# Optimization experiments

Measured on AMD Instinct MI355X. Metric: run time of the kernel, lower is better.

The kernel has to match this reference:

```python
import jax, jax.numpy as jnp
import numpy as np

D = 1024      # input_dim
H = 4096      # expert_hidden_dim
C = 512       # num_classes
E = 8         # num_experts
K = 2         # top_k
B = 16384     # batch
LN_EPS = 1e-5


def setup_inputs() -> dict:
    key = jax.random.key(0)
    ks = jax.random.split(key, 6)
    scale = 0.02
    return {
        "x": jax.random.normal(ks[0], (B, D), dtype=jnp.float32),
        "gate_w": jax.random.normal(ks[1], (D, E), dtype=jnp.float32) * scale,
        "gate_b": jnp.zeros((E,), dtype=jnp.float32),
        "w1": jax.random.normal(ks[2], (E, D, H), dtype=jnp.float32) * scale,
        "b1": jnp.zeros((E, H), dtype=jnp.float32),
        "ln_g": jnp.ones((E, H), dtype=jnp.float32),
        "ln_b": jnp.zeros((E, H), dtype=jnp.float32),
        "w2": jax.random.normal(ks[3], (E, H, C), dtype=jnp.float32) * scale,
        "b2": jnp.zeros((E, C), dtype=jnp.float32),
    }


def reference(x, gate_w, gate_b, w1, b1, ln_g, ln_b, w2, b2):
    # Router: logits [B,E], top-k over experts, softmax over the k selected logits
    logits = x @ gate_w + gate_b
    top_vals, top_idx = jax.lax.top_k(logits, K)        # [B,K]
    probs = jax.nn.softmax(top_vals, axis=1)            # [B,K]

    # Combined gate weight per (token, expert): replaces the nested k/expert
    # mask-gather-scatter loops; top_idx rows have distinct experts, so this
    # is exactly sum_k probs[:,k] * (top_idx[:,k]==e). [B,E]
    n = x.shape[0]
    weight = jnp.zeros((n, E), dtype=x.dtype).at[jnp.arange(n)[:, None], top_idx].add(probs)

    out = jnp.zeros((n, C), dtype=x.dtype)
    for e in range(E):  # fixed small expert count; each expert has distinct params
        h = x @ w1[e] + b1[e]                           # [B,H]
        mu = jnp.mean(h, axis=-1, keepdims=True)
        var = jnp.var(h, axis=-1, keepdims=True)
        h = (h - mu) * jax.lax.rsqrt(var + LN_EPS) * ln_g[e] + ln_b[e]
        h = jax.nn.gelu(h, approximate=False)           # torch GELU default = erf
        # Dropout is identity in eval mode.
        out = out + weight[:, e:e + 1] * (h @ w2[e] + b2[e])
    return out, logits
```

## Files before the change

kernel.cpp:

```cpp
#include <hip/hip_runtime.h>
#include <hip/hip_bf16.h>
#include <cstdint>

#define DEV __device__ __forceinline__

constexpr int Bt = 16384;
constexpr int Dd = 1024;
constexpr int Hh = 4096;
constexpr int Cc = 512;
constexpr int Ee = 8;
constexpr int PCAP = 34816;

typedef short bf16x8 __attribute__((ext_vector_type(8)));
typedef ushort u16x8 __attribute__((ext_vector_type(8)));
typedef float f32x4  __attribute__((ext_vector_type(4)));

DEV ushort f2bf(float f){
  uint32_t u = __float_as_uint(f);
  u += 0x7fffu + ((u >> 16) & 1u);
  return (ushort)(u >> 16);
}
DEV float bf2f(ushort u){ return __uint_as_float(((uint32_t)u) << 16); }

DEV float gelu_t(float x){
  float x2 = x * x;
  float z = x * (0.7978845608f + 0.0356774081f * x2);
  float t = __builtin_amdgcn_exp2f(z * -2.8853900818f);
  return x * __builtin_amdgcn_rcpf(1.f + t);
}

typedef const __attribute__((address_space(1))) void* gptr_t;
typedef __attribute__((address_space(3))) void* lptr_t;
DEV void gload_lds16(const void* g, void* l){
  __builtin_amdgcn_global_load_lds((gptr_t)g, (lptr_t)l, 16, 0, 0);
}

#define BARRIER() __builtin_amdgcn_s_barrier()
#define WAITL(N) do { asm volatile("s_waitcnt lgkmcnt(" #N ")" ::: "memory"); \
                      __builtin_amdgcn_sched_barrier(0); } while(0)
#define WAITV(N) asm volatile("s_waitcnt vmcnt(" #N ")" ::: "memory")

__global__ __launch_bounds__(256) void k_router(
    const float* __restrict__ x, const float* __restrict__ gw,
    const float* __restrict__ gb, float* __restrict__ logits,
    int2* __restrict__ topi, float2* __restrict__ topp)
{
  __shared__ float lgwT[Ee * Dd];
  int tid = threadIdx.x;
  const float4* gw4 = (const float4*)gw;
  for (int i = tid; i < Dd * Ee / 4; i += 256){
    float4 v = gw4[i];
    int d = i >> 1, e0 = (i & 1) * 4;
    lgwT[(e0 + 0) * Dd + d] = v.x;
    lgwT[(e0 + 1) * Dd + d] = v.y;
    lgwT[(e0 + 2) * Dd + d] = v.z;
    lgwT[(e0 + 3) * Dd + d] = v.w;
  }
  __syncthreads();
  int wv = tid >> 6, lane = tid & 63;
  int t = blockIdx.x * 4 + wv;
  const float* xr = x + (size_t)t * Dd;
  float acc[Ee];
  #pragma unroll
  for (int e = 0; e < Ee; e++) acc[e] = 0.f;
  for (int i = 0; i < Dd / 64; i++){
    int d = i * 64 + lane;
    float xs = xr[d];
    #pragma unroll
    for (int e = 0; e < Ee; e++) acc[e] += xs * lgwT[e * Dd + d];
  }
  #pragma unroll
  for (int e = 0; e < Ee; e++){
    #pragma unroll
    for (int m = 1; m < 64; m <<= 1) acc[e] += __shfl_xor(acc[e], m, 64);
  }
  if (lane == 0){
    float lg[Ee];
    #pragma unroll
    for (int e = 0; e < Ee; e++) lg[e] = acc[e] + gb[e];
    #pragma unroll
    for (int e = 0; e < Ee; e++) logits[(size_t)t * Ee + e] = lg[e];
    int i0 = 0; float v0 = lg[0];
    #pragma unroll
    for (int e = 1; e < Ee; e++) if (lg[e] > v0){ v0 = lg[e]; i0 = e; }
    int i1 = (i0 == 0) ? 1 : 0; float v1 = lg[i1];
    #pragma unroll
    for (int e = 0; e < Ee; e++) if (e != i0 && lg[e] > v1){ v1 = lg[e]; i1 = e; }
    float ex = expf(v1 - v0);
    float p0 = 1.f / (1.f + ex);
    float p1 = ex * p0;
    topi[t] = make_int2(i0, i1);
    topp[t] = make_float2(p0, p1);
  }
}

__global__ __launch_bounds__(256) void k_offsets(
    const int2* __restrict__ topi, int* __restrict__ off)
{
  __shared__ int part[4][8];
  int tid = threadIdx.x, lane = tid & 63, w = tid >> 6;
  int c0 = 0, c1 = 0, c2 = 0, c3 = 0, c4 = 0, c5 = 0, c6 = 0, c7 = 0;
  for (int t = tid; t < Bt; t += 256){
    int2 ii = topi[t];
    c0 += (ii.x == 0) + (ii.y == 0);
    c1 += (ii.x == 1) + (ii.y == 1);
    c2 += (ii.x == 2) + (ii.y == 2);
    c3 += (ii.x == 3) + (ii.y == 3);
    c4 += (ii.x == 4) + (ii.y == 4);
    c5 += (ii.x == 5) + (ii.y == 5);
    c6 += (ii.x == 6) + (ii.y == 6);
    c7 += (ii.x == 7) + (ii.y == 7);
  }
  #pragma unroll
  for (int m = 1; m < 64; m <<= 1){
    c0 += __shfl_xor(c0, m, 64); c1 += __shfl_xor(c1, m, 64);
    c2 += __shfl_xor(c2, m, 64); c3 += __shfl_xor(c3, m, 64);
    c4 += __shfl_xor(c4, m, 64); c5 += __shfl_xor(c5, m, 64);
    c6 += __shfl_xor(c6, m, 64); c7 += __shfl_xor(c7, m, 64);
  }
  if (lane == 0){
    part[w][0] = c0; part[w][1] = c1; part[w][2] = c2; part[w][3] = c3;
    part[w][4] = c4; part[w][5] = c5; part[w][6] = c6; part[w][7] = c7;
  }
  __syncthreads();
  if (tid == 0){
    int a = 0;
    for (int e = 0; e < Ee; e++){
      int h = part[0][e] + part[1][e] + part[2][e] + part[3][e];
      off[e] = a; a += ((h + 255) >> 8) << 8;
    }
    off[Ee] = a;
  }
}

__global__ __launch_bounds__(256) void k_scatter(
    const int2* __restrict__ topi, const int* __restrict__ off,
    int* __restrict__ fill, int* __restrict__ ptok, int2* __restrict__ pidx)
{
  __shared__ int lcnt[8], lbase[8];
  int tid = threadIdx.x;
  if (tid < 8) lcnt[tid] = 0;
  __syncthreads();
  int t = blockIdx.x * 256 + tid;
  int2 ii = topi[t];
  int r0 = atomicAdd(&lcnt[ii.x], 1);
  int r1 = atomicAdd(&lcnt[ii.y], 1);
  __syncthreads();
  if (tid < 8) lbase[tid] = off[tid] + atomicAdd(&fill[tid], lcnt[tid]);
  __syncthreads();
  int p0 = lbase[ii.x] + r0;
  int p1 = lbase[ii.y] + r1;
  ptok[p0] = t;
  ptok[p1] = t;
  pidx[t] = make_int2(p0, p1);
}

__global__ __launch_bounds__(256) void k_cvt_bf16(
    const float* __restrict__ in, ushort* __restrict__ outp, int n4)
{
  int i = blockIdx.x * 256 + threadIdx.x;
  if (i >= n4) return;
  float4 v = ((const float4*)in)[i];
  ushort4 o; o.x = f2bf(v.x); o.y = f2bf(v.y); o.z = f2bf(v.z); o.w = f2bf(v.w);
  ((ushort4*)outp)[i] = o;
}

__global__ __launch_bounds__(256) void k_transpose_bf16(
    const float* __restrict__ in, ushort* __restrict__ outp, int R, int Cd)
{
  __shared__ float tl[64][65];
  size_t eoff = (size_t)blockIdx.z * (size_t)R * (size_t)Cd;
  int c0 = blockIdx.x * 64, r0 = blockIdx.y * 64;
  int tid = threadIdx.x;
  int r = tid >> 2, cq = tid & 3;
  const float* src = in + eoff + (size_t)(r0 + r) * Cd + c0 + cq * 16;
  #pragma unroll
  for (int q = 0; q < 4; q++){
    float4 v = ((const float4*)src)[q];
    int cc = cq * 16 + q * 4;
    tl[r][cc + 0] = v.x; tl[r][cc + 1] = v.y; tl[r][cc + 2] = v.z; tl[r][cc + 3] = v.w;
  }
  __syncthreads();
  int c = tid >> 2, rq = tid & 3;
  ushort* dst = outp + eoff + (size_t)(c0 + c) * R + r0 + rq * 16;
  #pragma unroll
  for (int q = 0; q < 4; q++){
    ushort4 o;
    o.x = f2bf(tl[rq * 16 + q * 4 + 0][c]);
    o.y = f2bf(tl[rq * 16 + q * 4 + 1][c]);
    o.z = f2bf(tl[rq * 16 + q * 4 + 2][c]);
    o.w = f2bf(tl[rq * 16 + q * 4 + 3][c]);
    ((ushort4*)dst)[q] = o;
  }
}


DEV void read_Aq(bf16x8 (&aq)[4][2], const char* lb, int abase, const uint32_t (&alane)[2]){
  #pragma unroll
  for (int i = 0; i < 4; i++)
    #pragma unroll
    for (int k2 = 0; k2 < 2; k2++)
      aq[i][k2] = *(const bf16x8*)(lb + abase + i * 2048 + alane[k2]);
}
template<int P>
DEV void read_Bp(bf16x8 (&bq)[4][2], const char* lb, int wn, const uint32_t (&alane)[2]){
  #pragma unroll
  for (int j = 0; j < 2; j++)
    #pragma unroll
    for (int k2 = 0; k2 < 2; k2++)
      bq[P * 2 + j][k2] = *(const bf16x8*)(lb + 32768 + (wn >> 1) * 16384 +
                              (wn & 1) * 8192 + P * 4096 + j * 2048 + alane[k2]);
}
template<int MQ, int NB>
DEV void mfma_half(f32x4 (&acc)[8][4], const bf16x8 (&a)[4][2], const bf16x8 (&b)[4][2]){
  #pragma unroll
  for (int i = 0; i < 4; i++)
    #pragma unroll
    for (int j = 0; j < 2; j++)
      #pragma unroll
      for (int k2 = 0; k2 < 2; k2++)
        acc[MQ * 4 + i][NB * 2 + j] = __builtin_amdgcn_mfma_f32_16x16x32_bf16(
            a[i][k2], b[NB * 2 + j][k2], acc[MQ * 4 + i][NB * 2 + j], 0, 0, 0);
}
DEV void stage4(const char* gb, const uint32_t (&src)[2][2], uint32_t ko, char* dst){
  gload_lds16(gb + src[0][0] + ko, dst);
  gload_lds16(gb + src[0][1] + ko, dst + 8192);
  gload_lds16(gb + src[1][0] + ko, dst + 16384);
  gload_lds16(gb + src[1][1] + ko, dst + 16384 + 8192);
}

template<int MODE, int Kd, int Nd, int KS>
__global__ __launch_bounds__(512, 2) void k_gemm8(
    const ushort* __restrict__ A, const ushort* __restrict__ Bm,
    const float* __restrict__ bias, const int* __restrict__ off,
    const int* __restrict__ ptok, ushort* __restrict__ Outp, int chunk_base,
    int plane_elems)
{
  __shared__ char lds[131072];
  constexpr int Kh  = Kd / KS;
  constexpr int NTk = Kh / 64;
  constexpr int NTn = Nd / 256;
  int nwg = gridDim.x;
  int orig = blockIdx.x;
  int q = nwg >> 3, r8 = nwg & 7;
  int xcd = orig & 7, lin = orig >> 3;
  int swz = (xcd < r8 ? xcd * (q + 1) : r8 * (q + 1) + (xcd - r8) * q) + lin;
  int mcount = nwg / (NTn * KS);
  int m = swz % mcount;
  int rest = swz / mcount;
  int nI = rest % NTn, ksI = rest / NTn;
  int r0l = m * 256;
  int n0 = nI * 256;
  uint32_t kbyte = (uint32_t)ksI * (uint32_t)(Kh * 2);
  int grow0 = chunk_base + r0l;
  if (grow0 >= off[8]) return;

  int tid = threadIdx.x;
  int e = 0;
  #pragma unroll
  for (int i = 1; i < 8; i++) e = (grow0 >= off[i]) ? i : e;

  uint32_t sx = (uint32_t)(((tid & 7) ^ ((tid >> 3) & 7)) << 4);
  int rh0 = tid >> 3, rh1 = rh0 + 64;
  uint32_t a_src[2][2], b_src[2][2];
  #pragma unroll
  for (int h = 0; h < 2; h++){
    int ra0 = h * 128 + rh0, ra1 = h * 128 + rh1;
    uint32_t rowb0, rowb1;
    if (MODE == 0){
      rowb0 = (uint32_t)ptok[grow0 + ra0] * (uint32_t)(Kd * 2);
      rowb1 = (uint32_t)ptok[grow0 + ra1] * (uint32_t)(Kd * 2);
    } else {
      rowb0 = (uint32_t)(r0l + ra0) * (uint32_t)(Kd * 2);
      rowb1 = (uint32_t)(r0l + ra1) * (uint32_t)(Kd * 2);
    }
    a_src[h][0] = rowb0 + kbyte + sx;
    a_src[h][1] = rowb1 + kbyte + sx;
    b_src[h][0] = (uint32_t)(e * Nd + n0 + ra0) * (uint32_t)(Kd * 2) + kbyte + sx;
    b_src[h][1] = (uint32_t)(e * Nd + n0 + ra1) * (uint32_t)(Kd * 2) + kbyte + sx;
  }
  const char* Ab = (const char*)A;
  const char* Bb = (const char*)Bm;
  int w = tid >> 6, lane = tid & 63;
  int wm = w >> 2, wn = w & 3;
  int l15 = lane & 15, lhi = lane >> 4;
  char* wdst = lds + w * 1024;
  int abase0 = wm * 16384;
  int abase1 = wm * 16384 + 8192;

  uint32_t alane[2];
  #pragma unroll
  for (int k2 = 0; k2 < 2; k2++)
    alane[k2] = (uint32_t)(l15 * 128 + (((k2 * 4 + lhi) ^ (l15 & 7)) << 4));

  f32x4 acc[8][4];
  #pragma unroll
  for (int mi = 0; mi < 8; mi++)
    #pragma unroll
    for (int ni = 0; ni < 4; ni++) acc[mi][ni] = (f32x4){0.f, 0.f, 0.f, 0.f};
  bf16x8 aq[4][2], bq[4][2];

  stage4(Ab, a_src, 0u, wdst);
  stage4(Bb, b_src, 0u, wdst + 32768);
  stage4(Ab, a_src, 128u, wdst + 65536);
  stage4(Bb, b_src, 128u, wdst + 65536 + 32768);
  WAITV(8);
  BARRIER();
  read_Aq(aq, lds, abase0, alane);
  read_Bp<0>(bq, lds, wn, alane);
  read_Bp<1>(bq, lds, wn, alane);

  #pragma unroll 1
  for (int t = 0; t < NTk; ++t){
    const char* lb = lds + (t & 1) * 65536;
    char* wlb = wdst + (t & 1) * 65536;
    WAITL(4);
    __builtin_amdgcn_s_setprio(1);
    mfma_half<0, 0>(acc, aq, bq);
    __builtin_amdgcn_s_setprio(0);
    WAITL(0);
    __builtin_amdgcn_s_setprio(1);
    mfma_half<0, 1>(acc, aq, bq);
    __builtin_amdgcn_s_setprio(0);
    read_Aq(aq, lb, abase1, alane);
    WAITL(0);
    BARRIER();
    if (t + 2 < NTk){
      uint32_t ko2 = (uint32_t)(t + 2) * 128u;
      stage4(Ab, a_src, ko2, wlb);
      stage4(Bb, b_src, ko2, wlb + 32768);
    }
    __builtin_amdgcn_s_setprio(1);
    mfma_half<1, 1>(acc, aq, bq);
    mfma_half<1, 0>(acc, aq, bq);
    __builtin_amdgcn_s_setprio(0);
    if (t + 2 < NTk)      { WAITV(8); }
    else if (t + 1 < NTk) { WAITV(0); }
    BARRIER();
    if (t + 1 < NTk){
      const char* nb = lds + ((t + 1) & 1) * 65536;
      read_Aq(aq, nb, abase0, alane);
      read_Bp<0>(bq, nb, wn, alane);
      read_Bp<1>(bq, nb, wn, alane);
    }
  }

  float bv[4]; int nn[4];
  #pragma unroll
  for (int ni = 0; ni < 4; ni++){
    nn[ni] = n0 + wn * 64 + ni * 16 + l15;
    bv[ni] = (MODE == 0 || ksI == 0) ? bias[e * Nd + nn[ni]] : 0.f;
  }
  ushort* OutP = Outp + (size_t)ksI * (size_t)plane_elems;
  #pragma unroll
  for (int mi = 0; mi < 8; mi++){
    #pragma unroll
    for (int r = 0; r < 4; r++){
      int rl = r0l + wm * 128 + mi * 16 + lhi * 4 + r;
      size_t rowbase = (MODE == 0) ? (size_t)rl * Nd
                                   : (size_t)(chunk_base + rl) * Nd;
      #pragma unroll
      for (int ni = 0; ni < 4; ni++){
        float v = acc[mi][ni][r] + bv[ni];
        OutP[rowbase + nn[ni]] = f2bf(v);
      }
    }
  }
}

__global__ __launch_bounds__(256) void k_lngelu(
    ushort* __restrict__ h, const int* __restrict__ off,
    const float* __restrict__ lng, const float* __restrict__ lnb, int chunk_base)
{
  __shared__ float redS[8];
  int rl = blockIdx.x, tid = threadIdx.x;
  int grow = chunk_base + rl;
  if (grow >= off[8]) return;
  int e = 0;
  #pragma unroll
  for (int i = 1; i < 8; i++) e = (grow >= off[i]) ? i : e;
  ushort* hr = h + (size_t)rl * Hh;
  float xv[16];
  #pragma unroll
  for (int i = 0; i < 4; i++){
    int c = i * 256 + tid;
    ushort4 v = *(const ushort4*)(hr + c * 4);
    xv[i * 4 + 0] = bf2f(v.x); xv[i * 4 + 1] = bf2f(v.y);
    xv[i * 4 + 2] = bf2f(v.z); xv[i * 4 + 3] = bf2f(v.w);
  }
  float s0 = 0.f, s1 = 0.f;
  #pragma unroll
  for (int i = 0; i < 16; i++){ s0 += xv[i]; s1 += xv[i] * xv[i]; }
  #pragma unroll
  for (int m = 1; m < 64; m <<= 1){ s0 += __shfl_xor(s0, m, 64); s1 += __shfl_xor(s1, m, 64); }
  int w = tid >> 6;
  if ((tid & 63) == 0){ redS[w * 2] = s0; redS[w * 2 + 1] = s1; }
  __syncthreads();
  s0 = redS[0] + redS[2] + redS[4] + redS[6];
  s1 = redS[1] + redS[3] + redS[5] + redS[7];
  float mu = s0 * (1.f / 4096.f);
  float var = s1 * (1.f / 4096.f) - mu * mu;
  float rs = rsqrtf(var + 1e-5f);
  const float4* gp = (const float4*)(lng + (size_t)e * Hh);
  const float4* bp = (const float4*)(lnb + (size_t)e * Hh);
  #pragma unroll
  for (int i = 0; i < 4; i++){
    int c = i * 256 + tid;
    float4 g = gp[c], b = bp[c];
    float v0 = (xv[i * 4 + 0] - mu) * rs * g.x + b.x;
    float v1 = (xv[i * 4 + 1] - mu) * rs * g.y + b.y;
    float v2 = (xv[i * 4 + 2] - mu) * rs * g.z + b.z;
    float v3 = (xv[i * 4 + 3] - mu) * rs * g.w + b.w;
    ushort4 o;
    o.x = f2bf(gelu_t(v0)); o.y = f2bf(gelu_t(v1));
    o.z = f2bf(gelu_t(v2)); o.w = f2bf(gelu_t(v3));
    *(ushort4*)(hr + c * 4) = o;
  }
}

__global__ __launch_bounds__(128) void k_combine(
    const ushort* __restrict__ y, int plane, const int2* __restrict__ pidx,
    const float2* __restrict__ topp, float* __restrict__ outp)
{
  int t = blockIdx.x;
  int c4 = threadIdx.x << 2;
  int2 pi = pidx[t]; float2 pp = topp[t];
  ushort4 a0 = *(const ushort4*)(y + (size_t)pi.x * Cc + c4);
  ushort4 a1 = *(const ushort4*)(y + (size_t)plane + (size_t)pi.x * Cc + c4);
  ushort4 b0 = *(const ushort4*)(y + (size_t)pi.y * Cc + c4);
  ushort4 b1 = *(const ushort4*)(y + (size_t)plane + (size_t)pi.y * Cc + c4);
  float4 o;
  o.x = pp.x * (bf2f(a0.x) + bf2f(a1.x)) + pp.y * (bf2f(b0.x) + bf2f(b1.x));
  o.y = pp.x * (bf2f(a0.y) + bf2f(a1.y)) + pp.y * (bf2f(b0.y) + bf2f(b1.y));
  o.z = pp.x * (bf2f(a0.z) + bf2f(a1.z)) + pp.y * (bf2f(b0.z) + bf2f(b1.z));
  o.w = pp.x * (bf2f(a0.w) + bf2f(a1.w)) + pp.y * (bf2f(b0.w) + bf2f(b1.w));
  *(float4*)(outp + (size_t)t * Cc + c4) = o;
}

extern "C" void kernel_launch(void* const* d_in, const int* in_sizes, int n_in,
                              void* d_out, int out_size, void* d_ws, size_t ws_size,
                              hipStream_t stream)
{
  const float* x   = (const float*)d_in[0];
  const float* gw  = (const float*)d_in[1];
  const float* gb  = (const float*)d_in[2];
  const float* w1  = (const float*)d_in[3];
  const float* b1  = (const float*)d_in[4];
  const float* lng = (const float*)d_in[5];
  const float* lnb = (const float*)d_in[6];
  const float* w2  = (const float*)d_in[7];
  const float* b2  = (const float*)d_in[8];
  float* outp   = (float*)d_out;
  float* logits = outp + (size_t)Bt * Cc;

  constexpr int YPLANE = PCAP * Cc;

  char* p = (char*)d_ws;
  auto alloc = [&](size_t bytes) -> char* {
    char* q = p; p += (bytes + 255) & ~(size_t)255; return q;
  };
  int*    ctrl  = (int*)alloc(256);
  int* fill = ctrl + 8; int* off = ctrl + 16;
  int2*   topi  = (int2*)alloc((size_t)Bt * 8);
  float2* topp  = (float2*)alloc((size_t)Bt * 8);
  int2*   pidx  = (int2*)alloc((size_t)Bt * 8);
  int*    ptok  = (int*)alloc((size_t)PCAP * 4);
  ushort* ybuf  = (ushort*)alloc((size_t)YPLANE * 2 * 2);
  ushort* xb    = (ushort*)alloc((size_t)Bt * Dd * 2);
  ushort* w1t   = (ushort*)alloc((size_t)Ee * Hh * Dd * 2);
  ushort* w2t   = (ushort*)alloc((size_t)Ee * Cc * Hh * 2);
  size_t used  = (size_t)(p - (char*)d_ws);
  size_t avail = ws_size > used ? ws_size - used : 0;
  long long chr = (long long)(avail / ((size_t)Hh * 2));
  chr &= ~255LL;
  int CH = (int)(chr < 256 ? 256 : (chr > PCAP ? (long long)PCAP : chr));
  ushort* hbuf = (ushort*)p;

  hipMemsetAsync(ctrl, 0, 256, stream);
  hipMemsetAsync(ptok, 0, (size_t)PCAP * 4, stream);

  k_router<<<Bt / 4, 256, 0, stream>>>(x, gw, gb, logits, topi, topp);
  k_offsets<<<1, 256, 0, stream>>>(topi, off);
  k_scatter<<<Bt / 256, 256, 0, stream>>>(topi, off, fill, ptok, pidx);
  k_cvt_bf16<<<(Bt * Dd / 4) / 256, 256, 0, stream>>>(x, xb, Bt * Dd / 4);
  k_transpose_bf16<<<dim3(Hh / 64, Dd / 64, Ee), 256, 0, stream>>>(w1, w1t, Dd, Hh);
  k_transpose_bf16<<<dim3(Cc / 64, Hh / 64, Ee), 256, 0, stream>>>(w2, w2t, Hh, Cc);

  for (int base = 0; base < PCAP; base += CH){
    int rows = (PCAP - base < CH) ? (PCAP - base) : CH;
    int nb1 = (rows / 256) * (Hh / 256);
    k_gemm8<0, Dd, Hh, 1><<<nb1, 512, 0, stream>>>(xb, w1t, b1, off, ptok, hbuf, base, 0);
    k_lngelu<<<rows, 256, 0, stream>>>(hbuf, off, lng, lnb, base);
    int nb2 = (rows / 256) * (Cc / 256) * 2;
    k_gemm8<1, Hh, Cc, 2><<<nb2, 512, 0, stream>>>(hbuf, w2t, b2, off, ptok, ybuf, base, YPLANE);
  }
  k_combine<<<Bt, 128, 0, stream>>>(ybuf, YPLANE, pidx, topp, outp);
}
```

Before: 771.8 us.

## Simplify GEMM main loop: read LDS fragments at iteration start, drop manual waits

Restructures the double-buffered GEMM K-loop so that LDS fragment reads for the current tile happen at the top of each iteration instead of being prefetched for the next tile at the end of the previous one. The hand-placed lgkmcnt waits and s_setprio hints are removed, leaving the compiler to schedule the LDS reads against the MFMAs. The global-to-LDS staging of tile t+2 and its vmcnt wait now run after all four MFMA halves instead of overlapping with the second pair. The likely intent is to let the compiler find a better interleaving or to ease register pressure, at the cost of losing explicit LDS-read/MFMA overlap across iterations and overlap of the stage with compute.

```diff
diff --git a/kernel.cpp b/kernel.cpp
--- a/kernel.cpp
+++ b/kernel.cpp
@@ -36,8 +36,6 @@
 }
 
 #define BARRIER() __builtin_amdgcn_s_barrier()
-#define WAITL(N) do { asm volatile("s_waitcnt lgkmcnt(" #N ")" ::: "memory"); \
-                      __builtin_amdgcn_sched_barrier(0); } while(0)
 #define WAITV(N) asm volatile("s_waitcnt vmcnt(" #N ")" ::: "memory")
 
 __global__ __launch_bounds__(256) void k_router(
@@ -306,43 +304,31 @@
   stage4(Bb, b_src, 128u, wdst + 65536 + 32768);
   WAITV(8);
   BARRIER();
-  read_Aq(aq, lds, abase0, alane);
-  read_Bp<0>(bq, lds, wn, alane);
-  read_Bp<1>(bq, lds, wn, alane);
 
   #pragma unroll 1
   for (int t = 0; t < NTk; ++t){
     const char* lb = lds + (t & 1) * 65536;
     char* wlb = wdst + (t & 1) * 65536;
-    WAITL(4);
-    __builtin_amdgcn_s_setprio(1);
+    read_Aq(aq, lb, abase0, alane);
+    read_Bp<0>(bq, lb, wn, alane);
+    read_Bp<1>(bq, lb, wn, alane);
     mfma_half<0, 0>(acc, aq, bq);
-    __builtin_amdgcn_s_setprio(0);
-    WAITL(0);
-    __builtin_amdgcn_s_setprio(1);
     mfma_half<0, 1>(acc, aq, bq);
-    __builtin_amdgcn_s_setprio(0);
     read_Aq(aq, lb, abase1, alane);
-    WAITL(0);
+    mfma_half<1, 1>(acc, aq, bq);
+    mfma_half<1, 0>(acc, aq, bq);
+    asm volatile("s_waitcnt lgkmcnt(0)" ::: "memory");
+    __builtin_amdgcn_sched_barrier(0);
     BARRIER();
     if (t + 2 < NTk){
       uint32_t ko2 = (uint32_t)(t + 2) * 128u;
       stage4(Ab, a_src, ko2, wlb);
       stage4(Bb, b_src, ko2, wlb + 32768);
+      WAITV(8);
+    } else if (t + 1 < NTk) {
+      WAITV(0);
     }
-    __builtin_amdgcn_s_setprio(1);
-    mfma_half<1, 1>(acc, aq, bq);
-    mfma_half<1, 0>(acc, aq, bq);
-    __builtin_amdgcn_s_setprio(0);
-    if (t + 2 < NTk)      { WAITV(8); }
-    else if (t + 1 < NTk) { WAITV(0); }
     BARRIER();
-    if (t + 1 < NTk){
-      const char* nb = lds + ((t + 1) & 1) * 65536;
-      read_Aq(aq, nb, abase0, alane);
-      read_Bp<0>(bq, nb, wn, alane);
-      read_Bp<1>(bq, nb, wn, alane);
-    }
   }
 
   float bv[4]; int nn[4];
```

Result: slower. 804.7 us (+4.3%).

## Fuse LayerNorm+GELU apply into second GEMM A-load, keep only stats kernel

Applied to the files above, without the earlier changes.

Replaces the LN+GELU kernel, which read and rewrote the whole hidden buffer, with a small per-row stats kernel that only reads it. The second GEMM now loads the raw hidden tiles through registers, applies normalization and GELU, and writes bf16 to LDS instead of using direct global-to-LDS loads. This removes one full write pass over the hidden activations. In exchange the A operand goes through VGPRs with extra ALU work, including erf, inside the GEMM main loop. Each tile is also redone by both N-tiles, and this may hurt MFMA overlap. First-GEMM output stores become nontemporal.

```diff
diff --git a/kernel.cpp b/kernel.cpp
--- a/kernel.cpp
+++ b/kernel.cpp
@@ -194,6 +194,36 @@
   }
 }
 
+__global__ __launch_bounds__(256) void k_stats(
+    const ushort* __restrict__ h, const int* __restrict__ off,
+    float2* __restrict__ stats, int chunk_base)
+{
+  __shared__ float redS[8];
+  int rl = blockIdx.x, tid = threadIdx.x;
+  int grow = chunk_base + rl;
+  if (grow >= off[8]) return;
+  const ushort* hr = h + (size_t)rl * Hh;
+  float s0 = 0.f, s1 = 0.f;
+  #pragma unroll
+  for (int i = 0; i < 2; i++){
+    u16x8 v = *(const u16x8*)(hr + i * 2048 + tid * 8);
+    #pragma unroll
+    for (int j = 0; j < 8; j++){ float xx = bf2f((ushort)v[j]); s0 += xx; s1 += xx * xx; }
+  }
+  #pragma unroll
+  for (int m = 1; m < 64; m <<= 1){ s0 += __shfl_xor(s0, m, 64); s1 += __shfl_xor(s1, m, 64); }
+  int w = tid >> 6;
+  if ((tid & 63) == 0){ redS[w * 2] = s0; redS[w * 2 + 1] = s1; }
+  __syncthreads();
+  if (tid == 0){
+    s0 = redS[0] + redS[2] + redS[4] + redS[6];
+    s1 = redS[1] + redS[3] + redS[5] + redS[7];
+    float mu = s0 * (1.f / 4096.f);
+    float var = s1 * (1.f / 4096.f) - mu * mu;
+    stats[grow] = make_float2(mu, rsqrtf(var + 1e-5f));
+  }
+}
+
 
 DEV void read_Aq(bf16x8 (&aq)[4][2], const char* lb, int abase, const uint32_t (&alane)[2]){
   #pragma unroll
@@ -228,13 +258,26 @@
   gload_lds16(gb + src[1][0] + ko, dst + 16384);
   gload_lds16(gb + src[1][1] + ko, dst + 16384 + 8192);
 }
+DEV bf16x8 ln_gelu8(u16x8 hv, float2 st, float4 g0, float4 g1, float4 b0, float4 b1){
+  float gg[8] = {g0.x, g0.y, g0.z, g0.w, g1.x, g1.y, g1.z, g1.w};
+  float bb[8] = {b0.x, b0.y, b0.z, b0.w, b1.x, b1.y, b1.z, b1.w};
+  bf16x8 o;
+  #pragma unroll
+  for (int i = 0; i < 8; i++){
+    float xx = bf2f((ushort)hv[i]);
+    float v = (xx - st.x) * st.y * gg[i] + bb[i];
+    o[i] = (short)f2bf(gelu_t(v));
+  }
+  return o;
+}
 
 template<int MODE, int Kd, int Nd, int KS>
 __global__ __launch_bounds__(512, 2) void k_gemm8(
     const ushort* __restrict__ A, const ushort* __restrict__ Bm,
     const float* __restrict__ bias, const int* __restrict__ off,
-    const int* __restrict__ ptok, ushort* __restrict__ Outp, int chunk_base,
-    int plane_elems)
+    const int* __restrict__ ptok, const float2* __restrict__ stats,
+    const float* __restrict__ lng, const float* __restrict__ lnb,
+    ushort* __restrict__ Outp, int chunk_base, int plane_elems)
 {
   __shared__ char lds[131072];
   constexpr int Kh  = Kd / KS;
@@ -285,6 +328,7 @@
   int wm = w >> 2, wn = w & 3;
   int l15 = lane & 15, lhi = lane >> 4;
   char* wdst = lds + w * 1024;
+  uint32_t adst = (uint32_t)tid * 16u;
   int abase0 = wm * 16384;
   int abase1 = wm * 16384 + 8192;
 
@@ -293,6 +337,20 @@
   for (int k2 = 0; k2 < 2; k2++)
     alane[k2] = (uint32_t)(l15 * 128 + (((k2 * 4 + lhi) ^ (l15 & 7)) << 4));
 
+  float2 st00{}, st01{}, st10{}, st11{};
+  const float* gle = nullptr; const float* lbe = nullptr; int kglb = 0;
+  u16x8 h00{}, h01{}, h10{}, h11{};
+  float4 pg0{}, pg1{}, pb0{}, pb1{};
+  if constexpr (MODE == 1){
+    st00 = stats[grow0 + rh0];
+    st01 = stats[grow0 + rh1];
+    st10 = stats[grow0 + 128 + rh0];
+    st11 = stats[grow0 + 128 + rh1];
+    gle = lng + (size_t)e * Hh;
+    lbe = lnb + (size_t)e * Hh;
+    kglb = (int)(kbyte >> 1) + (int)(sx >> 1);
+  }
+
   f32x4 acc[8][4];
   #pragma unroll
   for (int mi = 0; mi < 8; mi++)
@@ -300,11 +358,43 @@
     for (int ni = 0; ni < 4; ni++) acc[mi][ni] = (f32x4){0.f, 0.f, 0.f, 0.f};
   bf16x8 aq[4][2], bq[4][2];
 
-  stage4(Ab, a_src, 0u, wdst);
-  stage4(Bb, b_src, 0u, wdst + 32768);
-  stage4(Ab, a_src, 128u, wdst + 65536);
-  stage4(Bb, b_src, 128u, wdst + 65536 + 32768);
-  WAITV(8);
+  if constexpr (MODE == 0){
+    stage4(Ab, a_src, 0u, wdst);
+    stage4(Bb, b_src, 0u, wdst + 32768);
+    stage4(Ab, a_src, 128u, wdst + 65536);
+    stage4(Bb, b_src, 128u, wdst + 65536 + 32768);
+    WAITV(8);
+  } else {
+    stage4(Bb, b_src, 0u, wdst + 32768);
+    stage4(Bb, b_src, 128u, wdst + 65536 + 32768);
+    #pragma unroll
+    for (int tt = 0; tt < 2; tt++){
+      uint32_t ko = (uint32_t)tt * 128u;
+      u16x8 r00 = *(const u16x8*)(Ab + a_src[0][0] + ko);
+      u16x8 r01 = *(const u16x8*)(Ab + a_src[0][1] + ko);
+      u16x8 r10 = *(const u16x8*)(Ab + a_src[1][0] + ko);
+      u16x8 r11 = *(const u16x8*)(Ab + a_src[1][1] + ko);
+      int kg = kglb + tt * 64;
+      float4 g0 = *(const float4*)(gle + kg), g1 = *(const float4*)(gle + kg + 4);
+      float4 c0 = *(const float4*)(lbe + kg), c1 = *(const float4*)(lbe + kg + 4);
+      char* ad = lds + tt * 65536;
+      *(bf16x8*)(ad + adst)         = ln_gelu8(r00, st00, g0, g1, c0, c1);
+      *(bf16x8*)(ad + adst + 8192)  = ln_gelu8(r01, st01, g0, g1, c0, c1);
+      *(bf16x8*)(ad + adst + 16384) = ln_gelu8(r10, st10, g0, g1, c0, c1);
+      *(bf16x8*)(ad + adst + 24576) = ln_gelu8(r11, st11, g0, g1, c0, c1);
+    }
+    if (NTk > 2){
+      h00 = *(const u16x8*)(Ab + a_src[0][0] + 256u);
+      h01 = *(const u16x8*)(Ab + a_src[0][1] + 256u);
+      h10 = *(const u16x8*)(Ab + a_src[1][0] + 256u);
+      h11 = *(const u16x8*)(Ab + a_src[1][1] + 256u);
+      int kg = kglb + 128;
+      pg0 = *(const float4*)(gle + kg); pg1 = *(const float4*)(gle + kg + 4);
+      pb0 = *(const float4*)(lbe + kg); pb1 = *(const float4*)(lbe + kg + 4);
+    }
+    WAITV(8);
+    WAITL(0);
+  }
   BARRIER();
   read_Aq(aq, lds, abase0, alane);
   read_Bp<0>(bq, lds, wn, alane);
@@ -325,17 +415,45 @@
     read_Aq(aq, lb, abase1, alane);
     WAITL(0);
     BARRIER();
-    if (t + 2 < NTk){
-      uint32_t ko2 = (uint32_t)(t + 2) * 128u;
-      stage4(Ab, a_src, ko2, wlb);
-      stage4(Bb, b_src, ko2, wlb + 32768);
+    uint32_t ko2 = (uint32_t)(t + 2) * 128u;
+    bool wrote = false;
+    if constexpr (MODE == 0){
+      if (t + 2 < NTk){
+        stage4(Ab, a_src, ko2, wlb);
+        stage4(Bb, b_src, ko2, wlb + 32768);
+      }
+    } else {
+      if (t + 2 < NTk){
+        stage4(Bb, b_src, ko2, wlb + 32768);
+        char* ad = lds + (t & 1) * 65536;
+        *(bf16x8*)(ad + adst)         = ln_gelu8(h00, st00, pg0, pg1, pb0, pb1);
+        *(bf16x8*)(ad + adst + 8192)  = ln_gelu8(h01, st01, pg0, pg1, pb0, pb1);
+        *(bf16x8*)(ad + adst + 16384) = ln_gelu8(h10, st10, pg0, pg1, pb0, pb1);
+        *(bf16x8*)(ad + adst + 24576) = ln_gelu8(h11, st11, pg0, pg1, pb0, pb1);
+        wrote = true;
+        if (t + 3 < NTk){
+          uint32_t ko3 = ko2 + 128u;
+          h00 = *(const u16x8*)(Ab + a_src[0][0] + ko3);
+          h01 = *(const u16x8*)(Ab + a_src[0][1] + ko3);
+          h10 = *(const u16x8*)(Ab + a_src[1][0] + ko3);
+          h11 = *(const u16x8*)(Ab + a_src[1][1] + ko3);
+          int kg3 = kglb + (int)(ko3 >> 1);
+          pg0 = *(const float4*)(gle + kg3); pg1 = *(const float4*)(gle + kg3 + 4);
+          pb0 = *(const float4*)(lbe + kg3); pb1 = *(const float4*)(lbe + kg3 + 4);
+        }
+      }
     }
     __builtin_amdgcn_s_setprio(1);
     mfma_half<1, 1>(acc, aq, bq);
     mfma_half<1, 0>(acc, aq, bq);
     __builtin_amdgcn_s_setprio(0);
-    if (t + 2 < NTk)      { WAITV(8); }
-    else if (t + 1 < NTk) { WAITV(0); }
+    if constexpr (MODE == 0){
+      if (t + 2 < NTk)      { WAITV(8); }
+      else if (t + 1 < NTk) { WAITV(0); }
+    } else {
+      if (wrote)            { WAITL(0); }
+      else if (t + 1 < NTk) { WAITV(0); }
+    }
     BARRIER();
     if (t + 1 < NTk){
       const char* nb = lds + ((t + 1) & 1) * 65536;
@@ -362,59 +480,9 @@
       #pragma unroll
       for (int ni = 0; ni < 4; ni++){
         float v = acc[mi][ni][r] + bv[ni];
-        OutP[rowbase + nn[ni]] = f2bf(v);
+        __builtin_nontemporal_store(f2bf(v), &OutP[rowbase + nn[ni]]);
       }
     }
-  }
-}
-
-__global__ __launch_bounds__(256) void k_lngelu(
-    ushort* __restrict__ h, const int* __restrict__ off,
-    const float* __restrict__ lng, const float* __restrict__ lnb, int chunk_base)
-{
-  __shared__ float redS[8];
-  int rl = blockIdx.x, tid = threadIdx.x;
-  int grow = chunk_base + rl;
-  if (grow >= off[8]) return;
-  int e = 0;
-  #pragma unroll
-  for (int i = 1; i < 8; i++) e = (grow >= off[i]) ? i : e;
-  ushort* hr = h + (size_t)rl * Hh;
-  float xv[16];
-  #pragma unroll
-  for (int i = 0; i < 4; i++){
-    int c = i * 256 + tid;
-    ushort4 v = *(const ushort4*)(hr + c * 4);
-    xv[i * 4 + 0] = bf2f(v.x); xv[i * 4 + 1] = bf2f(v.y);
-    xv[i * 4 + 2] = bf2f(v.z); xv[i * 4 + 3] = bf2f(v.w);
-  }
-  float s0 = 0.f, s1 = 0.f;
-  #pragma unroll
-  for (int i = 0; i < 16; i++){ s0 += xv[i]; s1 += xv[i] * xv[i]; }
-  #pragma unroll
-  for (int m = 1; m < 64; m <<= 1){ s0 += __shfl_xor(s0, m, 64); s1 += __shfl_xor(s1, m, 64); }
-  int w = tid >> 6;
-  if ((tid & 63) == 0){ redS[w * 2] = s0; redS[w * 2 + 1] = s1; }
-  __syncthreads();
-  s0 = redS[0] + redS[2] + redS[4] + redS[6];
-  s1 = redS[1] + redS[3] + redS[5] + redS[7];
-  float mu = s0 * (1.f / 4096.f);
-  float var = s1 * (1.f / 4096.f) - mu * mu;
-  float rs = rsqrtf(var + 1e-5f);
-  const float4* gp = (const float4*)(lng + (size_t)e * Hh);
-  const float4* bp = (const float4*)(lnb + (size_t)e * Hh);
-  #pragma unroll
-  for (int i = 0; i < 4; i++){
-    int c = i * 256 + tid;
-    float4 g = gp[c], b = bp[c];
-    float v0 = (xv[i * 4 + 0] - mu) * rs * g.x + b.x;
-    float v1 = (xv[i * 4 + 1] - mu) * rs * g.y + b.y;
-    float v2 = (xv[i * 4 + 2] - mu) * rs * g.z + b.z;
-    float v3 = (xv[i * 4 + 3] - mu) * rs * g.w + b.w;
-    ushort4 o;
-    o.x = f2bf(gelu_t(v0)); o.y = f2bf(gelu_t(v1));
-    o.z = f2bf(gelu_t(v2)); o.w = f2bf(gelu_t(v3));
-    *(ushort4*)(hr + c * 4) = o;
   }
 }
 
@@ -465,6 +533,7 @@
   float2* topp  = (float2*)alloc((size_t)Bt * 8);
   int2*   pidx  = (int2*)alloc((size_t)Bt * 8);
   int*    ptok  = (int*)alloc((size_t)PCAP * 4);
+  float2* stats = (float2*)alloc((size_t)PCAP * 8);
   ushort* ybuf  = (ushort*)alloc((size_t)YPLANE * 2 * 2);
   ushort* xb    = (ushort*)alloc((size_t)Bt * Dd * 2);
   ushort* w1t   = (ushort*)alloc((size_t)Ee * Hh * Dd * 2);
@@ -489,10 +558,12 @@
   for (int base = 0; base < PCAP; base += CH){
     int rows = (PCAP - base < CH) ? (PCAP - base) : CH;
     int nb1 = (rows / 256) * (Hh / 256);
-    k_gemm8<0, Dd, Hh, 1><<<nb1, 512, 0, stream>>>(xb, w1t, b1, off, ptok, hbuf, base, 0);
-    k_lngelu<<<rows, 256, 0, stream>>>(hbuf, off, lng, lnb, base);
+    k_gemm8<0, Dd, Hh, 1><<<nb1, 512, 0, stream>>>(
+        xb, w1t, b1, off, ptok, stats, lng, lnb, hbuf, base, 0);
+    k_stats<<<rows, 256, 0, stream>>>(hbuf, off, stats, base);
     int nb2 = (rows / 256) * (Cc / 256) * 2;
-    k_gemm8<1, Hh, Cc, 2><<<nb2, 512, 0, stream>>>(hbuf, w2t, b2, off, ptok, ybuf, base, YPLANE);
+    k_gemm8<1, Hh, Cc, 2><<<nb2, 512, 0, stream>>>(
+        hbuf, w2t, b2, off, ptok, stats, lng, lnb, ybuf, base, YPLANE);
   }
   k_combine<<<Bt, 128, 0, stream>>>(ybuf, YPLANE, pidx, topp, outp);
 }
```

Measured after the change: 1.198 ms. 1.55x slower.

## Fuse bf16 conversion of x into router and reorder GEMM tile swizzle

Applied to the files above, without the earlier changes.

The router kernel now reads x as float4, writes the bf16 copy of x as it goes, and computes the gate logits from the same registers. This removes the separate conversion kernel and a second full read of x. The GEMM block-index mapping also changes so that consecutive swizzled blocks iterate over N tiles and K splits of the same row block instead of over row blocks. That changes L2 reuse: the A rows are shared across neighbouring blocks, while the B tiles are reused less.

```diff
diff --git a/kernel.cpp b/kernel.cpp
--- a/kernel.cpp
+++ b/kernel.cpp
@@ -40,10 +40,10 @@
                       __builtin_amdgcn_sched_barrier(0); } while(0)
 #define WAITV(N) asm volatile("s_waitcnt vmcnt(" #N ")" ::: "memory")
 
-__global__ __launch_bounds__(256) void k_router(
+__global__ __launch_bounds__(256) void k_routercvt(
     const float* __restrict__ x, const float* __restrict__ gw,
     const float* __restrict__ gb, float* __restrict__ logits,
-    int2* __restrict__ topi, float2* __restrict__ topp)
+    int2* __restrict__ topi, float2* __restrict__ topp, ushort* __restrict__ xb)
 {
   __shared__ float lgwT[Ee * Dd];
   int tid = threadIdx.x;
@@ -59,15 +59,22 @@
   __syncthreads();
   int wv = tid >> 6, lane = tid & 63;
   int t = blockIdx.x * 4 + wv;
-  const float* xr = x + (size_t)t * Dd;
+  const float4* xr4 = (const float4*)(x + (size_t)t * Dd);
+  ushort* xbr = xb + (size_t)t * Dd;
   float acc[Ee];
   #pragma unroll
   for (int e = 0; e < Ee; e++) acc[e] = 0.f;
-  for (int i = 0; i < Dd / 64; i++){
-    int d = i * 64 + lane;
-    float xs = xr[d];
-    #pragma unroll
-    for (int e = 0; e < Ee; e++) acc[e] += xs * lgwT[e * Dd + d];
+  #pragma unroll
+  for (int i = 0; i < 4; i++){
+    int d4 = i * 256 + lane * 4;
+    float4 xs = xr4[d4 >> 2];
+    ushort4 o; o.x = f2bf(xs.x); o.y = f2bf(xs.y); o.z = f2bf(xs.z); o.w = f2bf(xs.w);
+    *(ushort4*)(xbr + d4) = o;
+    #pragma unroll
+    for (int e = 0; e < Ee; e++){
+      float4 wv4 = *(const float4*)(lgwT + e * Dd + d4);
+      acc[e] += xs.x * wv4.x + xs.y * wv4.y + xs.z * wv4.z + xs.w * wv4.w;
+    }
   }
   #pragma unroll
   for (int e = 0; e < Ee; e++){
@@ -155,16 +162,6 @@
   pidx[t] = make_int2(p0, p1);
 }
 
-__global__ __launch_bounds__(256) void k_cvt_bf16(
-    const float* __restrict__ in, ushort* __restrict__ outp, int n4)
-{
-  int i = blockIdx.x * 256 + threadIdx.x;
-  if (i >= n4) return;
-  float4 v = ((const float4*)in)[i];
-  ushort4 o; o.x = f2bf(v.x); o.y = f2bf(v.y); o.z = f2bf(v.z); o.w = f2bf(v.w);
-  ((ushort4*)outp)[i] = o;
-}
-
 __global__ __launch_bounds__(256) void k_transpose_bf16(
     const float* __restrict__ in, ushort* __restrict__ outp, int R, int Cd)
 {
@@ -245,10 +242,9 @@
   int q = nwg >> 3, r8 = nwg & 7;
   int xcd = orig & 7, lin = orig >> 3;
   int swz = (xcd < r8 ? xcd * (q + 1) : r8 * (q + 1) + (xcd - r8) * q) + lin;
-  int mcount = nwg / (NTn * KS);
-  int m = swz % mcount;
-  int rest = swz / mcount;
-  int nI = rest % NTn, ksI = rest / NTn;
+  int inner = swz % (NTn * KS);
+  int m = swz / (NTn * KS);
+  int nI = inner % NTn, ksI = inner / NTn;
   int r0l = m * 256;
   int n0 = nI * 256;
   uint32_t kbyte = (uint32_t)ksI * (uint32_t)(Kh * 2);
@@ -479,10 +475,9 @@
   hipMemsetAsync(ctrl, 0, 256, stream);
   hipMemsetAsync(ptok, 0, (size_t)PCAP * 4, stream);
 
-  k_router<<<Bt / 4, 256, 0, stream>>>(x, gw, gb, logits, topi, topp);
+  k_routercvt<<<Bt / 4, 256, 0, stream>>>(x, gw, gb, logits, topi, topp, xb);
   k_offsets<<<1, 256, 0, stream>>>(topi, off);
   k_scatter<<<Bt / 256, 256, 0, stream>>>(topi, off, fill, ptok, pidx);
-  k_cvt_bf16<<<(Bt * Dd / 4) / 256, 256, 0, stream>>>(x, xb, Bt * Dd / 4);
   k_transpose_bf16<<<dim3(Hh / 64, Dd / 64, Ee), 256, 0, stream>>>(w1, w1t, Dd, Hh);
   k_transpose_bf16<<<dim3(Cc / 64, Hh / 64, Ee), 256, 0, stream>>>(w2, w2t, Hh, Cc);
 
```

Result: no change. 771.7 us (-0.0%).
